# Kernel optimization log

Hardware: AMD Instinct MI355X
Metric: run time of the kernel (lower is better)

## Reference

```python
import jax, jax.numpy as jnp
import numpy as np
import math

# Dimensions (see shape_source)
B, C, NH = 4, 256, 8
VP, VW = 6, 16   # vertical: patches-per-window (outer), windows (inner)
HP, HW = 32, 3   # horizontal: patches-per-window (outer), windows (inner)
NW, P = VW * HW, VP * HP   # 48 windows, 192 patches per window
GRID = 96                   # patch grid is 96x96
SHIFT = (HP // 2, VP // 2)  # (16, 3) = (window_shape[0]//2, window_shape[1]//2)
FF = 4 * C
SCALE = 1.0 / math.sqrt(C)  # source divides by sqrt(embedding_dim), not head_dim


def setup_inputs() -> dict:
    key = jax.random.key(0)
    ks = jax.random.split(key, 17)
    std = 0.02
    n = lambda k, s: (jax.random.normal(k, s, dtype=jnp.float32) * std)
    return {
        "embeddings": jax.random.normal(ks[0], (B, GRID, GRID, C), dtype=jnp.float32),
        "ln1_g": jnp.ones((C,), jnp.float32), "ln1_b": jnp.zeros((C,), jnp.float32),
        "wq": n(ks[1], (C, C)), "bq": jnp.zeros((C,), jnp.float32),
        "wk": n(ks[2], (C, C)), "bk": jnp.zeros((C,), jnp.float32),
        "wv": n(ks[3], (C, C)), "bv": jnp.zeros((C,), jnp.float32),
        "pos_bias": n(ks[4], (NH, P, P)),
        "ln2_g": jnp.ones((C,), jnp.float32), "ln2_b": jnp.zeros((C,), jnp.float32),
        "w1": n(ks[5], (C, FF)), "b1": jnp.zeros((FF,), jnp.float32),
        "w2": n(ks[6], (FF, C)), "b2": jnp.zeros((C,), jnp.float32),
    }


def _ln(x, g, b, eps=1e-5):
    m = jnp.mean(x, axis=-1, keepdims=True)
    v = jnp.mean(jnp.square(x - m), axis=-1, keepdims=True)
    return (x - m) * jax.lax.rsqrt(v + eps) * g + b


def reference(embeddings, ln1_g, ln1_b, wq, bq, wk, bk, wv, bv, pos_bias,
              ln2_g, ln2_b, w1, b1, w2, b2):
    x = jnp.roll(embeddings, SHIFT, axis=(1, 2))
    # part: H=(VP outer, VW inner), W=(HP outer, HW inner) -> [B, NW, P, C]
    p = x.reshape(B, VP, VW, HP, HW, C).transpose(0, 2, 4, 1, 3, 5).reshape(B, NW, P, C)
    y = _ln(p, ln1_g, ln1_b)
    def heads(w, b):
        return (y @ w + b).reshape(B, NW, P, NH, C // NH).transpose(0, 1, 3, 2, 4)
    q, k, v = heads(wq, bq), heads(wk, bk), heads(wv, bv)  # [B, NW, NH, P, Dh]
    logits = jnp.einsum('bwhpd,bwhqd->bwhpq', q, k) * SCALE + pos_bias
    attn = jax.nn.softmax(logits, axis=-1)
    sa = jnp.einsum('bwhpq,bwhqd->bwhpd', attn, v)
    sa = sa.transpose(0, 1, 3, 2, 4).reshape(B, NW, P, C)
    a = p + sa
    h = _ln(a, ln2_g, ln2_b)
    ff = jax.nn.gelu(h @ w1 + b1, approximate=False) @ w2 + b2
    out = a + ff
    # join: inverse of part
    o = out.reshape(B, VW, HW, VP, HP, C).transpose(0, 3, 1, 4, 2, 5).reshape(B, GRID, GRID, C)
    return jnp.roll(o, (-SHIFT[0], -SHIFT[1]), axis=(1, 2))
```

## Files before the change

kernel.cpp:

```cpp
#include <hip/hip_runtime.h>
#include <hip/hip_bf16.h>
#include <cstdint>

using bf16x8 = __attribute__((ext_vector_type(8))) short;
using f32x4  = __attribute__((ext_vector_type(4))) float;
using bf16_t = __hip_bfloat16;

#define DEVI static __device__ __forceinline__

constexpr int kB = 4, kC = 256, kNH = 8, kDh = 32;
constexpr int kVP = 6, kVW = 16, kHP = 32, kHW = 3;
constexpr int kNW = 48, kP = 192, kGRID = 96;
constexpr int kRows = kB * kNW * kP;
constexpr int kFF = 1024;
constexpr float kScale = 0.0625f;

DEVI void row_coords(int row, int& b, int& g1, int& g2) {
  int b_  = row / (kNW * kP);
  int rem = row - b_ * (kNW * kP);
  int w = rem / kP;
  int p = rem - w * kP;
  int vw = w / kHW, hw = w - vw * kHW;
  int vp = p >> 5,  hp = p & 31;
  int r  = vp * kVW + vw;
  int cc = hp * kHW + hw;
  g1 = r + 80;  if (g1 >= kGRID) g1 -= kGRID;
  g2 = cc + 93; if (g2 >= kGRID) g2 -= kGRID;
  b = b_;
}

DEVI float bf2f(short s) {
  union { unsigned u; float f; } c;
  c.u = ((unsigned)(unsigned short)s) << 16;
  return c.f;
}
DEVI short f2bf(float f) {
  bf16_t h = __float2bfloat16(f);
  return *reinterpret_cast<short*>(&h);
}

DEVI void gload16(const void* g, void* l) {
  __builtin_amdgcn_global_load_lds(
      (__attribute__((address_space(1))) void*)(uintptr_t)g,
      (__attribute__((address_space(3))) void*)(uintptr_t)l, 16, 0, 0);
}

__global__ __launch_bounds__(256) void k_wconv(
    const float* __restrict__ wq, const float* __restrict__ wk,
    const float* __restrict__ wv, const float* __restrict__ w1,
    const float* __restrict__ w2, bf16_t* __restrict__ W) {
  const int i = blockIdx.x * 256 + threadIdx.x;
  if (i < 196608) {
    const int n = i >> 8, k = i & 255;
    const float* src = n < 256 ? wq : (n < 512 ? wk : wv);
    W[i] = __float2bfloat16(src[k * 256 + (n & 255)]);
  } else if (i < 458752) {
    const int j = i - 196608;
    const int n = j >> 8, k = j & 255;
    W[i] = __float2bfloat16(w1[k * 1024 + n]);
  } else if (i < 720896) {
    const int j = i - 458752;
    const int n = j >> 10, k = j & 1023;
    W[i] = __float2bfloat16(w2[k * 256 + n]);
  }
}

__global__ __launch_bounds__(256) void k_ln1(const float* __restrict__ emb,
    const float* __restrict__ gam, const float* __restrict__ bet,
    bf16_t* __restrict__ Y) {
  const int wave = threadIdx.x >> 6, lane = threadIdx.x & 63;
  #pragma unroll
  for (int rr = 0; rr < 2; ++rr) {
    const int row = blockIdx.x * 8 + wave * 2 + rr;
    int b, g1, g2; row_coords(row, b, g1, g2);
    const float* src = emb + (((size_t)b * kGRID + g1) * kGRID + g2) * kC;
    float4 x = *reinterpret_cast<const float4*>(src + lane * 4);
    float s  = x.x + x.y + x.z + x.w;
    float sq = x.x*x.x + x.y*x.y + x.z*x.z + x.w*x.w;
    #pragma unroll
    for (int off = 32; off; off >>= 1) { s += __shfl_xor(s, off); sq += __shfl_xor(sq, off); }
    const float mean = s * (1.f / kC);
    const float rstd = rsqrtf(sq * (1.f / kC) - mean * mean + 1e-5f);
    const float4 g4 = *reinterpret_cast<const float4*>(gam + lane * 4);
    const float4 b4 = *reinterpret_cast<const float4*>(bet + lane * 4);
    short4 o;
    o.x = f2bf((x.x - mean) * rstd * g4.x + b4.x);
    o.y = f2bf((x.y - mean) * rstd * g4.y + b4.y);
    o.z = f2bf((x.z - mean) * rstd * g4.z + b4.z);
    o.w = f2bf((x.w - mean) * rstd * g4.w + b4.w);
    *reinterpret_cast<short4*>(Y + (size_t)row * kC + lane * 4) = o;
  }
}

__global__ __launch_bounds__(256) void k_ln2(const float* __restrict__ emb,
    const bf16_t* __restrict__ SA,
    const float* __restrict__ gam, const float* __restrict__ bet,
    float* __restrict__ A, bf16_t* __restrict__ H) {
  const int wave = threadIdx.x >> 6, lane = threadIdx.x & 63;
  #pragma unroll
  for (int rr = 0; rr < 2; ++rr) {
    const int row = blockIdx.x * 8 + wave * 2 + rr;
    int b, g1, g2; row_coords(row, b, g1, g2);
    const float* src = emb + (((size_t)b * kGRID + g1) * kGRID + g2) * kC;
    float4 x = *reinterpret_cast<const float4*>(src + lane * 4);
    short4 sv = *reinterpret_cast<const short4*>(SA + (size_t)row * kC + lane * 4);
    x.x += bf2f(sv.x); x.y += bf2f(sv.y); x.z += bf2f(sv.z); x.w += bf2f(sv.w);
    *reinterpret_cast<float4*>(A + (size_t)row * kC + lane * 4) = x;
    float s  = x.x + x.y + x.z + x.w;
    float sq = x.x*x.x + x.y*x.y + x.z*x.z + x.w*x.w;
    #pragma unroll
    for (int off = 32; off; off >>= 1) { s += __shfl_xor(s, off); sq += __shfl_xor(sq, off); }
    const float mean = s * (1.f / kC);
    const float rstd = rsqrtf(sq * (1.f / kC) - mean * mean + 1e-5f);
    const float4 g4 = *reinterpret_cast<const float4*>(gam + lane * 4);
    const float4 b4 = *reinterpret_cast<const float4*>(bet + lane * 4);
    short4 o;
    o.x = f2bf((x.x - mean) * rstd * g4.x + b4.x);
    o.y = f2bf((x.y - mean) * rstd * g4.y + b4.y);
    o.z = f2bf((x.z - mean) * rstd * g4.z + b4.z);
    o.w = f2bf((x.w - mean) * rstd * g4.w + b4.w);
    *reinterpret_cast<short4*>(H + (size_t)row * kC + lane * 4) = o;
  }
}

template <int KDIM, int EPI>
__global__ __launch_bounds__(256) void k_gemm(
    const bf16_t* __restrict__ Amat, const bf16_t* __restrict__ BT,
    const float* __restrict__ bias0, const float* __restrict__ bias1,
    const float* __restrict__ bias2,
    bf16_t* __restrict__ Obf, const float* __restrict__ Ares,
    float* __restrict__ Out) {
  __shared__ bf16_t As[128 * 32];
  __shared__ bf16_t Bs[128 * 32];
  const int tid = threadIdx.x;
  const int wave = tid >> 6, lane = tid & 63;
  const int lr = lane & 15, kg = lane >> 4;
  const int m0 = blockIdx.x * 128, n0 = blockIdx.y * 128;
  const int wm = (wave >> 1) * 64, wn = (wave & 1) * 64;
  const int srow = lane >> 2, scol = (lane & 3) * 8;
  f32x4 acc[4][4] = {};
  for (int k0 = 0; k0 < KDIM; k0 += 32) {
    #pragma unroll
    for (int ic = 0; ic < 2; ++ic) {
      const int ch = wave * 2 + ic;
      const int row = ch * 16 + srow;
      gload16(Amat + (size_t)(m0 + row) * KDIM + k0 + scol, &As[ch * 512]);
      gload16(BT   + (size_t)(n0 + row) * KDIM + k0 + scol, &Bs[ch * 512]);
    }
    __syncthreads();
    bf16x8 af[4], bq[4];
    #pragma unroll
    for (int m = 0; m < 4; ++m)
      af[m] = *reinterpret_cast<const bf16x8*>(&As[(wm + m * 16 + lr) * 32 + kg * 8]);
    #pragma unroll
    for (int n = 0; n < 4; ++n)
      bq[n] = *reinterpret_cast<const bf16x8*>(&Bs[(wn + n * 16 + lr) * 32 + kg * 8]);
    #pragma unroll
    for (int m = 0; m < 4; ++m)
      #pragma unroll
      for (int n = 0; n < 4; ++n)
        acc[m][n] = __builtin_amdgcn_mfma_f32_16x16x32_bf16(af[m], bq[n], acc[m][n], 0, 0, 0);
    __syncthreads();
  }
  #pragma unroll
  for (int m = 0; m < 4; ++m) {
    #pragma unroll
    for (int n = 0; n < 4; ++n) {
      #pragma unroll
      for (int r = 0; r < 4; ++r) {
        const int row = m0 + wm + m * 16 + kg * 4 + r;
        const int col = n0 + wn + n * 16 + lr;
        float v = acc[m][n][r];
        if constexpr (EPI == 0) {
          const int which = col >> 8, c = col & 255;
          const float* bp = which == 0 ? bias0 : (which == 1 ? bias1 : bias2);
          v += bp[c];
          Obf[(size_t)which * kRows * kC + (size_t)row * kC + c] = __float2bfloat16(v);
        } else if constexpr (EPI == 1) {
          v += bias0[col];
          const float gl = 0.5f * v * (1.f + erff(v * 0.70710678118654752f));
          Obf[(size_t)row * kFF + col] = __float2bfloat16(gl);
        } else {
          v += bias0[col] + Ares[(size_t)row * kC + col];
          int b, g1, g2; row_coords(row, b, g1, g2);
          Out[(((size_t)b * kGRID + g1) * kGRID + g2) * kC + col] = v;
        }
      }
    }
  }
}

constexpr int kKsPad = 40;
constexpr int kVtPad = 200;
constexpr int kPlPad = 200;
__global__ __launch_bounds__(256) void k_attn(
    const bf16_t* __restrict__ Q, const bf16_t* __restrict__ K,
    const bf16_t* __restrict__ V, const float* __restrict__ pos,
    bf16_t* __restrict__ SA) {
  __shared__ short Ks[kP * kKsPad];
  __shared__ short Vt[kDh * kVtPad];
  __shared__ short Pl[4 * 16 * kPlPad];
  const int bw = blockIdx.x >> 3, h = blockIdx.x & 7;
  const int rowbase = bw * kP, colbase = h * kDh;
  const int tid = threadIdx.x, wave = tid >> 6, lane = tid & 63;
  const int lr = lane & 15, kg = lane >> 4;
  const int wq0 = wave * 48;
  const float* pb = pos + (size_t)h * kP * kP;

  #pragma unroll
  for (int i = 0; i < 3; ++i) {
    const int c = tid + i * 256;
    const int row = c >> 2, dch = (c & 3) * 8;
    const size_t gbase = (size_t)(rowbase + row) * kC + colbase + dch;
    bf16x8 kv = *reinterpret_cast<const bf16x8*>(K + gbase);
    *reinterpret_cast<bf16x8*>(&Ks[row * kKsPad + dch]) = kv;
    bf16x8 vv = *reinterpret_cast<const bf16x8*>(V + gbase);
    #pragma unroll
    for (int e = 0; e < 8; ++e) Vt[(dch + e) * kVtPad + row] = vv[e];
  }
  __syncthreads();

  for (int m = 0; m < 3; ++m) {
    const int rbase = wq0 + m * 16;
    bf16x8 aq = *reinterpret_cast<const bf16x8*>(
        Q + (size_t)(rowbase + rbase + lr) * kC + colbase + kg * 8);
    f32x4 s[12];
    #pragma unroll
    for (int n = 0; n < 12; ++n) {
      bf16x8 bk = *reinterpret_cast<const bf16x8*>(&Ks[(n * 16 + lr) * kKsPad + kg * 8]);
      s[n] = __builtin_amdgcn_mfma_f32_16x16x32_bf16(aq, bk, (f32x4){0.f, 0.f, 0.f, 0.f}, 0, 0, 0);
    }
    float mx[4] = {-1e30f, -1e30f, -1e30f, -1e30f};
    #pragma unroll
    for (int n = 0; n < 12; ++n) {
      #pragma unroll
      for (int r = 0; r < 4; ++r) {
        const float lg = fmaf(s[n][r], kScale,
                              pb[(size_t)(rbase + kg * 4 + r) * kP + n * 16 + lr]);
        s[n][r] = lg;
        mx[r] = fmaxf(mx[r], lg);
      }
    }
    #pragma unroll
    for (int r = 0; r < 4; ++r)
      #pragma unroll
      for (int off = 8; off; off >>= 1) mx[r] = fmaxf(mx[r], __shfl_xor(mx[r], off));
    float sm[4] = {0.f, 0.f, 0.f, 0.f};
    #pragma unroll
    for (int n = 0; n < 12; ++n)
      #pragma unroll
      for (int r = 0; r < 4; ++r) {
        const float e = __expf(s[n][r] - mx[r]);
        s[n][r] = e;
        sm[r] += e;
      }
    #pragma unroll
    for (int r = 0; r < 4; ++r) {
      #pragma unroll
      for (int off = 8; off; off >>= 1) sm[r] += __shfl_xor(sm[r], off);
      sm[r] = 1.f / sm[r];
    }
    #pragma unroll
    for (int n = 0; n < 12; ++n)
      #pragma unroll
      for (int r = 0; r < 4; ++r)
        Pl[(wave * 16 + kg * 4 + r) * kPlPad + n * 16 + lr] = f2bf(s[n][r] * sm[r]);
    f32x4 o0 = {0.f, 0.f, 0.f, 0.f}, o1 = {0.f, 0.f, 0.f, 0.f};
    #pragma unroll
    for (int kk = 0; kk < 6; ++kk) {
      bf16x8 ap = *reinterpret_cast<const bf16x8*>(&Pl[(wave * 16 + lr) * kPlPad + kk * 32 + kg * 8]);
      bf16x8 b0 = *reinterpret_cast<const bf16x8*>(&Vt[lr * kVtPad + kk * 32 + kg * 8]);
      bf16x8 b1 = *reinterpret_cast<const bf16x8*>(&Vt[(16 + lr) * kVtPad + kk * 32 + kg * 8]);
      o0 = __builtin_amdgcn_mfma_f32_16x16x32_bf16(ap, b0, o0, 0, 0, 0);
      o1 = __builtin_amdgcn_mfma_f32_16x16x32_bf16(ap, b1, o1, 0, 0, 0);
    }
    bf16_t* sp = SA + (size_t)(rowbase + rbase + kg * 4) * kC + colbase;
    #pragma unroll
    for (int r = 0; r < 4; ++r) {
      sp[(size_t)r * kC + lr]      = __float2bfloat16(o0[r]);
      sp[(size_t)r * kC + 16 + lr] = __float2bfloat16(o1[r]);
    }
  }
}

extern "C" void kernel_launch(void* const* d_in, const int* in_sizes, int n_in,
                              void* d_out, int out_size, void* d_ws, size_t ws_size,
                              hipStream_t stream) {
  const float* emb  = (const float*)d_in[0];
  const float* ln1g = (const float*)d_in[1];
  const float* ln1b = (const float*)d_in[2];
  const float* wq   = (const float*)d_in[3];
  const float* bq   = (const float*)d_in[4];
  const float* wk   = (const float*)d_in[5];
  const float* bk   = (const float*)d_in[6];
  const float* wv   = (const float*)d_in[7];
  const float* bv   = (const float*)d_in[8];
  const float* pos  = (const float*)d_in[9];
  const float* ln2g = (const float*)d_in[10];
  const float* ln2b = (const float*)d_in[11];
  const float* w1   = (const float*)d_in[12];
  const float* b1   = (const float*)d_in[13];
  const float* w2   = (const float*)d_in[14];
  const float* b2   = (const float*)d_in[15];

  char* ws = (char*)d_ws;
  const size_t nYb = (size_t)kRows * kC * 2;
  bf16_t* Y    = (bf16_t*)(ws);
  bf16_t* Qb   = (bf16_t*)(ws + nYb);
  bf16_t* SAb  = (bf16_t*)(ws + nYb * 4);
  float*  Abuf = (float*) (ws + nYb * 5);
  bf16_t* H    = (bf16_t*)(ws + nYb * 5 + (size_t)kRows * kC * 4);
  bf16_t* G    = (bf16_t*)(ws);
  bf16_t* W    = (bf16_t*)(ws + nYb * 5 + (size_t)kRows * kC * 4 + nYb);
  bf16_t* WqkvT = W;
  bf16_t* W1T   = W + 768 * 256;
  bf16_t* W2T   = W1T + 1024 * 256;

  k_wconv<<<2816, 256, 0, stream>>>(wq, wk, wv, w1, w2, W);
  k_ln1<<<kRows / 8, 256, 0, stream>>>(emb, ln1g, ln1b, Y);
  k_gemm<256, 0><<<dim3(kRows / 128, 6), 256, 0, stream>>>(
      Y, WqkvT, bq, bk, bv, Qb, nullptr, nullptr);
  k_attn<<<kB * kNW * kNH, 256, 0, stream>>>(
      Qb, Qb + (size_t)kRows * kC, Qb + 2 * (size_t)kRows * kC, pos, SAb);
  k_ln2<<<kRows / 8, 256, 0, stream>>>(emb, SAb, ln2g, ln2b, Abuf, H);
  k_gemm<256, 1><<<dim3(kRows / 128, 8), 256, 0, stream>>>(
      H, W1T, b1, nullptr, nullptr, G, nullptr, nullptr);
  k_gemm<1024, 2><<<dim3(kRows / 128, 2), 256, 0, stream>>>(
      G, W2T, b2, nullptr, nullptr, nullptr, Abuf, (float*)d_out);
}
```

Baseline: 201.6 us.

## Double-buffer GEMM LDS tiles, swizzle LDS layout, and reorder grid for reuse

```diff
diff --git a/kernel.cpp b/kernel.cpp
--- a/kernel.cpp
+++ b/kernel.cpp
@@ -130,37 +130,50 @@
     const float* __restrict__ bias2,
     bf16_t* __restrict__ Obf, const float* __restrict__ Ares,
     float* __restrict__ Out) {
-  __shared__ bf16_t As[128 * 32];
-  __shared__ bf16_t Bs[128 * 32];
+  __shared__ bf16_t As[2][128 * 32];
+  __shared__ bf16_t Bs[2][128 * 32];
   const int tid = threadIdx.x;
   const int wave = tid >> 6, lane = tid & 63;
   const int lr = lane & 15, kg = lane >> 4;
-  const int m0 = blockIdx.x * 128, n0 = blockIdx.y * 128;
+  const int m0 = blockIdx.y * 128, n0 = blockIdx.x * 128;
   const int wm = (wave >> 1) * 64, wn = (wave & 1) * 64;
-  const int srow = lane >> 2, scol = (lane & 3) * 8;
+  const int srow = lane >> 2;
+  const int scol = (((lane & 3) ^ (srow & 3)) << 3);
+  const int rdoff = ((kg ^ (lr & 3)) << 3);
+  const bf16_t* ga0 = Amat + (size_t)(m0 + (wave * 2) * 16 + srow) * KDIM + scol;
+  const bf16_t* gb0 = BT   + (size_t)(n0 + (wave * 2) * 16 + srow) * KDIM + scol;
+  const size_t rstep = (size_t)16 * KDIM;
+
   f32x4 acc[4][4] = {};
+  #pragma unroll
+  for (int ic = 0; ic < 2; ++ic) {
+    gload16(ga0 + ic * rstep, &As[0][(wave * 2 + ic) * 512]);
+    gload16(gb0 + ic * rstep, &Bs[0][(wave * 2 + ic) * 512]);
+  }
+  __syncthreads();
+  int buf = 0;
   for (int k0 = 0; k0 < KDIM; k0 += 32) {
-    #pragma unroll
-    for (int ic = 0; ic < 2; ++ic) {
-      const int ch = wave * 2 + ic;
-      const int row = ch * 16 + srow;
-      gload16(Amat + (size_t)(m0 + row) * KDIM + k0 + scol, &As[ch * 512]);
-      gload16(BT   + (size_t)(n0 + row) * KDIM + k0 + scol, &Bs[ch * 512]);
-    }
-    __syncthreads();
+    if (k0 + 32 < KDIM) {
+      #pragma unroll
+      for (int ic = 0; ic < 2; ++ic) {
+        gload16(ga0 + k0 + 32 + ic * rstep, &As[buf ^ 1][(wave * 2 + ic) * 512]);
+        gload16(gb0 + k0 + 32 + ic * rstep, &Bs[buf ^ 1][(wave * 2 + ic) * 512]);
+      }
+    }
     bf16x8 af[4], bq[4];
     #pragma unroll
     for (int m = 0; m < 4; ++m)
-      af[m] = *reinterpret_cast<const bf16x8*>(&As[(wm + m * 16 + lr) * 32 + kg * 8]);
+      af[m] = *reinterpret_cast<const bf16x8*>(&As[buf][(wm + m * 16 + lr) * 32 + rdoff]);
     #pragma unroll
     for (int n = 0; n < 4; ++n)
-      bq[n] = *reinterpret_cast<const bf16x8*>(&Bs[(wn + n * 16 + lr) * 32 + kg * 8]);
+      bq[n] = *reinterpret_cast<const bf16x8*>(&Bs[buf][(wn + n * 16 + lr) * 32 + rdoff]);
     #pragma unroll
     for (int m = 0; m < 4; ++m)
       #pragma unroll
       for (int n = 0; n < 4; ++n)
         acc[m][n] = __builtin_amdgcn_mfma_f32_16x16x32_bf16(af[m], bq[n], acc[m][n], 0, 0, 0);
     __syncthreads();
+    buf ^= 1;
   }
   #pragma unroll
   for (int m = 0; m < 4; ++m) {
@@ -318,13 +331,13 @@
 
   k_wconv<<<2816, 256, 0, stream>>>(wq, wk, wv, w1, w2, W);
   k_ln1<<<kRows / 8, 256, 0, stream>>>(emb, ln1g, ln1b, Y);
-  k_gemm<256, 0><<<dim3(kRows / 128, 6), 256, 0, stream>>>(
+  k_gemm<256, 0><<<dim3(6, kRows / 128), 256, 0, stream>>>(
       Y, WqkvT, bq, bk, bv, Qb, nullptr, nullptr);
   k_attn<<<kB * kNW * kNH, 256, 0, stream>>>(
       Qb, Qb + (size_t)kRows * kC, Qb + 2 * (size_t)kRows * kC, pos, SAb);
   k_ln2<<<kRows / 8, 256, 0, stream>>>(emb, SAb, ln2g, ln2b, Abuf, H);
-  k_gemm<256, 1><<<dim3(kRows / 128, 8), 256, 0, stream>>>(
+  k_gemm<256, 1><<<dim3(8, kRows / 128), 256, 0, stream>>>(
       H, W1T, b1, nullptr, nullptr, G, nullptr, nullptr);
-  k_gemm<1024, 2><<<dim3(kRows / 128, 2), 256, 0, stream>>>(
+  k_gemm<1024, 2><<<dim3(2, kRows / 128), 256, 0, stream>>>(
       G, W2T, b2, nullptr, nullptr, nullptr, Abuf, (float*)d_out);
 }
```

Result: slower. 209.1 us (+3.7%).

## Stage 256-wide K chunks in LDS with k-group-major layout for GEMM

Applied to the files above, without the earlier changes.

```diff
diff --git a/kernel.cpp b/kernel.cpp
--- a/kernel.cpp
+++ b/kernel.cpp
@@ -130,37 +130,42 @@
     const float* __restrict__ bias2,
     bf16_t* __restrict__ Obf, const float* __restrict__ Ares,
     float* __restrict__ Out) {
-  __shared__ bf16_t As[128 * 32];
-  __shared__ bf16_t Bs[128 * 32];
+  __shared__ bf16_t As[32 * 128 * 8];
+  __shared__ bf16_t Bs[32 * 128 * 8];
   const int tid = threadIdx.x;
   const int wave = tid >> 6, lane = tid & 63;
-  const int lr = lane & 15, kg = lane >> 4;
+  const int lr = lane & 15, kgf = lane >> 4;
   const int m0 = blockIdx.x * 128, n0 = blockIdx.y * 128;
   const int wm = (wave >> 1) * 64, wn = (wave & 1) * 64;
-  const int srow = lane >> 2, scol = (lane & 3) * 8;
   f32x4 acc[4][4] = {};
-  for (int k0 = 0; k0 < KDIM; k0 += 32) {
-    #pragma unroll
-    for (int ic = 0; ic < 2; ++ic) {
-      const int ch = wave * 2 + ic;
-      const int row = ch * 16 + srow;
-      gload16(Amat + (size_t)(m0 + row) * KDIM + k0 + scol, &As[ch * 512]);
-      gload16(BT   + (size_t)(n0 + row) * KDIM + k0 + scol, &Bs[ch * 512]);
+  for (int kc = 0; kc < KDIM; kc += 256) {
+    if (kc) __syncthreads();
+    #pragma unroll
+    for (int i = 0; i < 16; ++i) {
+      const int a = wave * 16 + i;
+      const int kg = a >> 1, rh = a & 1;
+      gload16(Amat + (size_t)(m0 + rh * 64 + lane) * KDIM + kc + kg * 8,
+              &As[(kg * 128 + rh * 64) * 8]);
+      gload16(BT   + (size_t)(n0 + rh * 64 + lane) * KDIM + kc + kg * 8,
+              &Bs[(kg * 128 + rh * 64) * 8]);
     }
     __syncthreads();
-    bf16x8 af[4], bq[4];
-    #pragma unroll
-    for (int m = 0; m < 4; ++m)
-      af[m] = *reinterpret_cast<const bf16x8*>(&As[(wm + m * 16 + lr) * 32 + kg * 8]);
-    #pragma unroll
-    for (int n = 0; n < 4; ++n)
-      bq[n] = *reinterpret_cast<const bf16x8*>(&Bs[(wn + n * 16 + lr) * 32 + kg * 8]);
-    #pragma unroll
-    for (int m = 0; m < 4; ++m)
+    #pragma unroll
+    for (int kk = 0; kk < 8; ++kk) {
+      const int kgg = kk * 4 + kgf;
+      bf16x8 af[4], bq[4];
+      #pragma unroll
+      for (int m = 0; m < 4; ++m)
+        af[m] = *reinterpret_cast<const bf16x8*>(&As[(kgg * 128 + wm + m * 16 + lr) * 8]);
       #pragma unroll
       for (int n = 0; n < 4; ++n)
-        acc[m][n] = __builtin_amdgcn_mfma_f32_16x16x32_bf16(af[m], bq[n], acc[m][n], 0, 0, 0);
-    __syncthreads();
+        bq[n] = *reinterpret_cast<const bf16x8*>(&Bs[(kgg * 128 + wn + n * 16 + lr) * 8]);
+      #pragma unroll
+      for (int m = 0; m < 4; ++m)
+        #pragma unroll
+        for (int n = 0; n < 4; ++n)
+          acc[m][n] = __builtin_amdgcn_mfma_f32_16x16x32_bf16(af[m], bq[n], acc[m][n], 0, 0, 0);
+    }
   }
   #pragma unroll
   for (int m = 0; m < 4; ++m) {
@@ -168,7 +173,7 @@
     for (int n = 0; n < 4; ++n) {
       #pragma unroll
       for (int r = 0; r < 4; ++r) {
-        const int row = m0 + wm + m * 16 + kg * 4 + r;
+        const int row = m0 + wm + m * 16 + kgf * 4 + r;
         const int col = n0 + wn + n * 16 + lr;
         float v = acc[m][n][r];
         if constexpr (EPI == 0) {
```

Measured after the change: 414.1 us. 2.05x slower.
